# Kernel tuning notes

Measured on AMD Instinct MI355X. Metric: run time of the kernel, lower is better.

## Reference

```python
import jax, jax.numpy as jnp
import numpy as np

N_NODES = 100000
N_EDGES = 1600000
N_GRAPHS = 2048
HID = 64
IN_F = 14
N_CLS = 2
EPS = 1e-5


def _gcn_conv(x, row, col, w_edge, W, b, n_nodes):
    # PyG GCNConv with add_self_loops=True, normalize=True.
    xw = x @ W  # [N, out]
    # degree on target nodes, self-loop contributes weight 1
    deg = jnp.zeros((n_nodes,), x.dtype).at[col].add(w_edge) + 1.0
    dinv = deg ** -0.5
    norm = dinv[row] * w_edge * dinv[col]  # [E]
    out = jnp.zeros_like(xw).at[col].add(norm[:, None] * xw[row])
    out = out + (dinv * dinv)[:, None] * xw  # self-loop term
    return out + b


def _bn_relu(x, gamma, beta):
    mean = jnp.mean(x, axis=0)
    var = jnp.var(x, axis=0)  # biased, as PyTorch BN training normalization
    y = gamma * (x - mean) * jax.lax.rsqrt(var + EPS) + beta
    return jax.nn.relu(y)


def setup_inputs() -> dict:
    key = jax.random.key(0)
    ks = jax.random.split(key, 8)
    x = jax.random.normal(ks[0], (N_NODES, IN_F), dtype=jnp.float32)
    edge_index = jax.random.randint(ks[1], (2, N_EDGES), 0, N_NODES, dtype=jnp.int64)
    batch = jnp.sort(jax.random.randint(ks[2], (N_NODES,), 0, N_GRAPHS, dtype=jnp.int64))
    edge_weight = jnp.ones((N_EDGES,), dtype=jnp.float32)
    def lin(k, fi, fo):
        s = 1.0 / np.sqrt(fi)
        kw, kb = jax.random.split(k)
        return (jax.random.uniform(kw, (fi, fo), jnp.float32, -s, s),
                jax.random.uniform(kb, (fo,), jnp.float32, -s, s))
    W1, b1 = lin(ks[3], IN_F, HID)
    W2, b2 = lin(ks[4], HID, HID)
    W3, b3 = lin(ks[5], HID, HID)
    fcW, fcb = lin(ks[6], HID, N_CLS)
    g = jnp.ones((HID,), jnp.float32)
    z = jnp.zeros((HID,), jnp.float32)
    return {
        "x": x, "edge_index": edge_index, "batch": batch, "edge_weight": edge_weight,
        "W1": W1, "b1": b1, "W2": W2, "b2": b2, "W3": W3, "b3": b3,
        "g1": g, "bt1": z, "g2": g, "bt2": z, "g3": g, "bt3": z,
        "fcW": fcW, "fcb": fcb,
    }


def reference(x, edge_index, batch, edge_weight, W1, b1, W2, b2, W3, b3,
              g1, bt1, g2, bt2, g3, bt3, fcW, fcb):
    row, col = edge_index[0], edge_index[1]
    n = x.shape[0]
    h = _bn_relu(_gcn_conv(x, row, col, edge_weight, W1, b1, n), g1, bt1)
    h = _bn_relu(_gcn_conv(h, row, col, edge_weight, W2, b2, n), g2, bt2)
    h = _bn_relu(_gcn_conv(h, row, col, edge_weight, W3, b3, n), g3, bt3)
    node_embs = h  # dropout p=0 is identity
    graph_emb = jax.ops.segment_sum(node_embs, batch, num_segments=N_GRAPHS)
    out = graph_emb @ fcW + fcb
    return (out, node_embs, graph_emb)
```

## Files before the change

### kernel.cpp

```cpp
#include <hip/hip_runtime.h>
#include <hip/hip_fp16.h>

#define N_NODES 100000
#define N_EDGES 1600000
#define EMAX4   1900000
#define N_GRAPHS 2048
#define HID 64
#define IN_F 14
#define N_CLS 2
#define EPS 1e-5f

#define BSHIFT 9
#define NBUCK 196
#define ABLOCKS 256
#define CHUNK (N_EDGES / ABLOCKS)

#define NBLK2 128
#define NCHUNK2 ((N_NODES + NBLK2 - 1) / NBLK2)

typedef _Float16 half_t;
typedef _Float16 half8 __attribute__((ext_vector_type(8)));
typedef float f32x4 __attribute__((ext_vector_type(4)));
typedef unsigned int u32;
typedef u32 u32x4 __attribute__((ext_vector_type(4)));
typedef u32 u32x2 __attribute__((ext_vector_type(2)));

#define GSTRIDE ((size_t)N_NODES * 16)

__device__ __forceinline__ __half2 u32_as_half2(u32 u) {
    union { u32 u; __half2 h; } c;
    c.u = u;
    return c.h;
}


__global__ __launch_bounds__(256) void histA_kernel(const int* __restrict__ col,
                                                    int* __restrict__ histG) {
    __shared__ int hl[NBUCK];
    for (int i = threadIdx.x; i < NBUCK; i += 256) hl[i] = 0;
    __syncthreads();
    int e0 = blockIdx.x * CHUNK;
    for (int e = e0 + threadIdx.x; e < e0 + CHUNK; e += 256)
        atomicAdd(&hl[col[e] >> BSHIFT], 1);
    __syncthreads();
    for (int i = threadIdx.x; i < NBUCK; i += 256)
        histG[i * ABLOCKS + blockIdx.x] = hl[i];
}

__global__ __launch_bounds__(256) void scanS1_kernel(const int* __restrict__ histG,
                                                     int* __restrict__ bsumA) {
    __shared__ int ls[256];
    ls[threadIdx.x] = histG[blockIdx.x * 256 + threadIdx.x];
    __syncthreads();
    for (int off = 128; off > 0; off >>= 1) {
        if (threadIdx.x < off) ls[threadIdx.x] += ls[threadIdx.x + off];
        __syncthreads();
    }
    if (threadIdx.x == 0) bsumA[blockIdx.x] = ls[0];
}

__global__ __launch_bounds__(512) void topscan_kernel(int* __restrict__ bsum, int nb) {
    __shared__ int ls[512];
    int t = threadIdx.x;
    int v = (t < nb) ? bsum[t] : 0;
    ls[t] = v;
    __syncthreads();
    for (int off = 1; off < 512; off <<= 1) {
        int x = ls[t];
        if (t >= off) x += ls[t - off];
        __syncthreads();
        ls[t] = x;
        __syncthreads();
    }
    if (t < nb) bsum[t] = ls[t] - v;
}

__global__ __launch_bounds__(256) void scanS3_kernel(int* __restrict__ histG,
                                                     const int* __restrict__ bsumA,
                                                     int* __restrict__ ptr) {
    __shared__ int ls[256];
    int idx = blockIdx.x * 256 + threadIdx.x;
    int v = histG[idx];
    ls[threadIdx.x] = v;
    __syncthreads();
    for (int off = 1; off < 256; off <<= 1) {
        int x = ls[threadIdx.x];
        if (threadIdx.x >= off) x += ls[threadIdx.x - off];
        __syncthreads();
        ls[threadIdx.x] = x;
        __syncthreads();
    }
    histG[idx] = ls[threadIdx.x] - v + bsumA[blockIdx.x];
    if (blockIdx.x == 0 && threadIdx.x == 0) ptr[N_NODES] = N_EDGES;
}

__global__ __launch_bounds__(256) void scatterA_kernel(const int* __restrict__ row,
                                                       const int* __restrict__ col,
                                                       const float* __restrict__ w,
                                                       const int* __restrict__ histG,
                                                       int2* __restrict__ EA) {
    __shared__ int cur[NBUCK];
    for (int i = threadIdx.x; i < NBUCK; i += 256)
        cur[i] = histG[i * ABLOCKS + blockIdx.x];
    __syncthreads();
    int e0 = blockIdx.x * CHUNK;
    for (int e = e0 + threadIdx.x; e < e0 + CHUNK; e += 256) {
        int c = col[e];
        int r = row[e];
        int fx = (int)__float2uint_rn(w[e] * 8192.0f);
        int pos = atomicAdd(&cur[c >> BSHIFT], 1);
        EA[pos] = make_int2(r, (fx << 17) | c);
    }
}

__global__ __launch_bounds__(256) void bucketA_kernel(const int2* __restrict__ EA,
                                                      const int* __restrict__ bsumA,
                                                      int* __restrict__ ptr,
                                                      float* __restrict__ dinv) {
    __shared__ int hist[512], wsum[512];
    int b = blockIdx.x;
    int beg = bsumA[b];
    int end = (b == NBUCK - 1) ? N_EDGES : bsumA[b + 1];
    int i0 = threadIdx.x, i1 = threadIdx.x + 256;
    hist[i0] = 0; hist[i1] = 0;
    wsum[i0] = 0; wsum[i1] = 0;
    __syncthreads();
    for (int e = beg + threadIdx.x; e < end; e += 256) {
        int2 ed = EA[e];
        int c9 = ed.y & 511;
        atomicAdd(&hist[c9], 1);
        atomicAdd(&wsum[c9], (int)((unsigned int)ed.y >> 17));
    }
    __syncthreads();
    int cnt0 = hist[i0], cnt1 = hist[i1];
    for (int off = 1; off < 512; off <<= 1) {
        int v0 = hist[i0], v1 = hist[i1];
        int a0 = (i0 >= off) ? hist[i0 - off] : 0;
        int a1 = (i1 >= off) ? hist[i1 - off] : 0;
        __syncthreads();
        hist[i0] = v0 + a0;
        hist[i1] = v1 + a1;
        __syncthreads();
    }
    int excl0 = hist[i0] - cnt0, excl1 = hist[i1] - cnt1;
    int col0 = (b << BSHIFT) + i0, col1 = (b << BSHIFT) + i1;
    if (col0 < N_NODES) {
        ptr[col0] = beg + excl0;
        dinv[col0] = rsqrtf(1.0f + (float)wsum[i0] * (1.0f / 8192.0f));
    }
    if (col1 < N_NODES) {
        ptr[col1] = beg + excl1;
        dinv[col1] = rsqrtf(1.0f + (float)wsum[i1] * (1.0f / 8192.0f));
    }
}


__global__ __launch_bounds__(256) void histD_kernel(const int* __restrict__ ptr,
                                                    int* __restrict__ histD) {
    __shared__ int hl[2048];
    for (int i = threadIdx.x; i < 2048; i += 256) hl[i] = 0;
    __syncthreads();
    int n0 = blockIdx.x * NCHUNK2;
    int n1 = n0 + NCHUNK2; if (n1 > N_NODES) n1 = N_NODES;
    for (int n = n0 + threadIdx.x; n < n1; n += 256) {
        int d = ptr[n + 1] - ptr[n];
        if (d > 255) d = 255;
        atomicAdd(&hl[((threadIdx.x & 7) << 8) + d], 1);
    }
    __syncthreads();
    int s = 0;
#pragma unroll
    for (int c = 0; c < 8; c++) s += hl[(c << 8) + threadIdx.x];
    histD[threadIdx.x * NBLK2 + blockIdx.x] = s;
}

__global__ __launch_bounds__(128) void scanD1_kernel(const int* __restrict__ histD,
                                                     int* __restrict__ rowTot) {
    __shared__ int ls[128];
    ls[threadIdx.x] = histD[blockIdx.x * NBLK2 + threadIdx.x];
    __syncthreads();
    for (int off = 64; off > 0; off >>= 1) {
        if (threadIdx.x < off) ls[threadIdx.x] += ls[threadIdx.x + off];
        __syncthreads();
    }
    if (threadIdx.x == 0) rowTot[blockIdx.x] = ls[0];
}

__global__ __launch_bounds__(256) void topscanD_kernel(const int* __restrict__ rowTot,
                                                       int* __restrict__ nodeExcl,
                                                       int* __restrict__ edgeExcl,
                                                       int* __restrict__ ptrS) {
    __shared__ int a[256], b[256];
    int t = threadIdx.x;
    int cnt = rowTot[t];
    int dpad = (t + 3) & ~3;
    int ec = cnt * dpad;
    a[t] = cnt; b[t] = ec;
    __syncthreads();
    for (int off = 1; off < 256; off <<= 1) {
        int va = a[t], vb = b[t];
        if (t >= off) { va += a[t - off]; vb += b[t - off]; }
        __syncthreads();
        a[t] = va; b[t] = vb;
        __syncthreads();
    }
    nodeExcl[t] = a[t] - cnt;
    edgeExcl[t] = b[t] - ec;
    if (t == 255) ptrS[N_NODES] = b[255];
}

__global__ __launch_bounds__(128) void scanD3_kernel(int* __restrict__ histD,
                                                     const int* __restrict__ nodeExcl) {
    __shared__ int ls[128];
    int idx = blockIdx.x * NBLK2 + threadIdx.x;
    int v = histD[idx];
    ls[threadIdx.x] = v;
    __syncthreads();
    for (int off = 1; off < 128; off <<= 1) {
        int x = ls[threadIdx.x];
        if (threadIdx.x >= off) x += ls[threadIdx.x - off];
        __syncthreads();
        ls[threadIdx.x] = x;
        __syncthreads();
    }
    histD[idx] = ls[threadIdx.x] - v + nodeExcl[blockIdx.x];
}

__global__ __launch_bounds__(256) void scatterD_kernel(const int* __restrict__ ptr,
                                                       const int* __restrict__ histD,
                                                       const int* __restrict__ nodeExcl,
                                                       const int* __restrict__ edgeExcl,
                                                       int* __restrict__ perm,
                                                       int* __restrict__ ptrS,
                                                       int* __restrict__ newbase) {
    __shared__ int cur[256];
    cur[threadIdx.x] = histD[threadIdx.x * NBLK2 + blockIdx.x];
    __syncthreads();
    int n0 = blockIdx.x * NCHUNK2;
    int n1 = n0 + NCHUNK2; if (n1 > N_NODES) n1 = N_NODES;
    for (int n = n0 + threadIdx.x; n < n1; n += 256) {
        int d = ptr[n + 1] - ptr[n];
        if (d > 255) d = 255;
        int dpad = (d + 3) & ~3;
        int pos = atomicAdd(&cur[d], 1);
        int ebase = edgeExcl[d] + (pos - nodeExcl[d]) * dpad;
        perm[pos] = n;
        ptrS[pos] = ebase;
        newbase[n] = ebase;
    }
}

__global__ __launch_bounds__(256) void bucketB_kernel(const int2* __restrict__ EA,
                                                      const int* __restrict__ bsumA,
                                                      const int* __restrict__ newbase,
                                                      const float* __restrict__ dinv,
                                                      unsigned int* __restrict__ srcoff,
                                                      half_t* __restrict__ normh) {
    __shared__ int cur[512];
    int b = blockIdx.x;
    int beg = bsumA[b];
    int end = (b == NBUCK - 1) ? N_EDGES : bsumA[b + 1];
    int i0 = threadIdx.x, i1 = threadIdx.x + 256;
    int col0 = (b << BSHIFT) + i0, col1 = (b << BSHIFT) + i1;
    cur[i0] = (col0 < N_NODES) ? newbase[col0] : 0;
    cur[i1] = (col1 < N_NODES) ? newbase[col1] : 0;
    __syncthreads();
    for (int e = beg + threadIdx.x; e < end; e += 256) {
        int2 ed = EA[e];
        int c = ed.y & 0x1ffff;
        float w = (float)((unsigned int)ed.y >> 17) * (1.0f / 8192.0f);
        float nrm = dinv[ed.x] * w * dinv[c];
        int pos = atomicAdd(&cur[c & 511], 1);
        srcoff[pos] = (unsigned int)ed.x << 5;
        normh[pos] = (half_t)nrm;
    }
}


template <int K>
__global__ __launch_bounds__(256) void gemm_kernel(const float* __restrict__ h,
                                                   const float* __restrict__ W,
                                                   half_t* __restrict__ xw, int n_nodes) {
    int f = threadIdx.x & 63;
    float wcol[K];
#pragma unroll
    for (int k = 0; k < K; k++) wcol[k] = W[k * HID + f];
    half_t* xg = xw + (size_t)(f >> 4) * GSTRIDE + (f & 15);
    int wave = (blockIdx.x * blockDim.x + threadIdx.x) >> 6;
    int nwaves = (gridDim.x * blockDim.x) >> 6;
    for (int n = wave; n < n_nodes; n += nwaves) {
        const float* hr = h + (size_t)n * K;
        float acc = 0.f;
#pragma unroll
        for (int k = 0; k < K; k++) acc += hr[k] * wcol[k];
        xg[(size_t)n * 16] = (half_t)acc;
    }
}

__global__ __launch_bounds__(256) void gemm_bn_mfma_kernel(const half_t* __restrict__ h,
                                                           const float* __restrict__ W,
                                                           const float* __restrict__ stats,
                                                           const float* __restrict__ gamma,
                                                           const float* __restrict__ beta,
                                                           half_t* __restrict__ xw, int n_nodes) {
    __shared__ float sc_s[HID], sh_s[HID];
    if (threadIdx.x < 64) {
        float mean = stats[threadIdx.x] * (1.0f / N_NODES);
        float var = stats[64 + threadIdx.x] * (1.0f / N_NODES) - mean * mean;
        float sc = gamma[threadIdx.x] * rsqrtf(var + EPS);
        sc_s[threadIdx.x] = sc;
        sh_s[threadIdx.x] = beta[threadIdx.x] - mean * sc;
    }
    __syncthreads();
    int lane = threadIdx.x & 63;
    int col16 = lane & 15;
    int quad = lane >> 4;

    float scA[2][8], shA[2][8];
#pragma unroll
    for (int kh = 0; kh < 2; kh++)
#pragma unroll
        for (int j = 0; j < 8; j++) {
            int k = kh * 32 + quad * 8 + j;
            scA[kh][j] = sc_s[k];
            shA[kh][j] = sh_s[k];
        }

    half8 bfrag[4][2];
#pragma unroll
    for (int t = 0; t < 4; t++)
#pragma unroll
        for (int kh = 0; kh < 2; kh++)
#pragma unroll
            for (int j = 0; j < 8; j++) {
                int k = kh * 32 + quad * 8 + j;
                bfrag[t][kh][j] = (half_t)W[k * HID + t * 16 + col16];
            }

    int wave = (blockIdx.x * blockDim.x + threadIdx.x) >> 6;
    int nwaves = (gridDim.x * blockDim.x) >> 6;
    int ntiles = n_nodes >> 4;
    for (int tIdx = wave; tIdx < ntiles; tIdx += nwaves) {
        int n0 = tIdx << 4;
        half8 afrag[2];
#pragma unroll
        for (int kh = 0; kh < 2; kh++) {
            int k0 = kh * 32 + quad * 8;
            const half_t* hp = h + (size_t)(k0 >> 4) * GSTRIDE
                                 + (size_t)(n0 + col16) * 16 + (k0 & 15);
            half8 raw = *(const half8*)hp;
#pragma unroll
            for (int j = 0; j < 8; j++) {
                float v = (float)raw[j] * scA[kh][j] + shA[kh][j];
                afrag[kh][j] = (half_t)fmaxf(v, 0.f);
            }
        }
        f32x4 acc[4];
#pragma unroll
        for (int t = 0; t < 4; t++) {
            f32x4 z = {0.f, 0.f, 0.f, 0.f};
            acc[t] = __builtin_amdgcn_mfma_f32_16x16x32_f16(afrag[0], bfrag[t][0], z, 0, 0, 0);
            acc[t] = __builtin_amdgcn_mfma_f32_16x16x32_f16(afrag[1], bfrag[t][1], acc[t], 0, 0, 0);
        }
#pragma unroll
        for (int t = 0; t < 4; t++) {
            half_t* xg = xw + (size_t)t * GSTRIDE;
#pragma unroll
            for (int r = 0; r < 4; r++) {
                int rowi = n0 + quad * 4 + r;
                xg[(size_t)rowi * 16 + col16] = (half_t)acc[t][r];
            }
        }
    }
}

template <bool LAST>
__global__ __launch_bounds__(256) void gather_stats_kernel(const int* __restrict__ ptrS,
                                                           const int* __restrict__ perm,
                                                           const unsigned int* __restrict__ srcoff,
                                                           const half_t* __restrict__ normh,
                                                           const half_t* __restrict__ xw,
                                                           const float* __restrict__ dinv,
                                                           const float* __restrict__ b,
                                                           half_t* __restrict__ hp,
                                                           float* __restrict__ hf,
                                                           float* __restrict__ stats,
                                                           int n_nodes) {
    int g = (blockIdx.x & 7) >> 1;
    int grank = ((blockIdx.x >> 3) << 1) | (blockIdx.x & 1);
    int lane16 = threadIdx.x & 15;
    int quadLocal = threadIdx.x >> 4;
    int quadId = grank * 16 + quadLocal;
    int nquads = (gridDim.x >> 2) * 16;

    const half_t* xg = xw + (size_t)g * GSTRIDE;
    const char* xgc = (const char*)xg;
    unsigned int loff = (unsigned int)(lane16 * 2);
    const unsigned int* np = (const unsigned int*)normh;
    half_t* hpg = hp + (size_t)g * GSTRIDE;
    int f = g * 16 + lane16;
    float bf = b[f];

    float s = 0.f, s2 = 0.f;
    for (int i = quadId; i < n_nodes; i += nquads) {
        int node = perm[i];
        int j = ptrS[i];
        int cend = ptrS[i + 1];
        __half2 z2 = __float2half2_rn(0.f);
        __half2 acc0 = z2, acc1 = z2, acc2 = z2, acc3 = z2;
        for (; j + 16 <= cend; j += 16) {
            u32x4 s0 = *(const u32x4*)(srcoff + j);
            u32x4 s1 = *(const u32x4*)(srcoff + j + 4);
            u32x4 s2v = *(const u32x4*)(srcoff + j + 8);
            u32x4 s3 = *(const u32x4*)(srcoff + j + 12);
            int jh = j >> 1;
            u32x2 n0 = *(const u32x2*)(np + jh);
            u32x2 n1 = *(const u32x2*)(np + jh + 2);
            u32x2 n2 = *(const u32x2*)(np + jh + 4);
            u32x2 n3 = *(const u32x2*)(np + jh + 6);
            __half h0 = *(const __half*)(xgc + (s0.x + loff));
            __half h1 = *(const __half*)(xgc + (s0.y + loff));
            __half h2 = *(const __half*)(xgc + (s0.z + loff));
            __half h3 = *(const __half*)(xgc + (s0.w + loff));
            __half h4 = *(const __half*)(xgc + (s1.x + loff));
            __half h5 = *(const __half*)(xgc + (s1.y + loff));
            __half h6 = *(const __half*)(xgc + (s1.z + loff));
            __half h7 = *(const __half*)(xgc + (s1.w + loff));
            __half h8 = *(const __half*)(xgc + (s2v.x + loff));
            __half h9 = *(const __half*)(xgc + (s2v.y + loff));
            __half hA = *(const __half*)(xgc + (s2v.z + loff));
            __half hB = *(const __half*)(xgc + (s2v.w + loff));
            __half hC = *(const __half*)(xgc + (s3.x + loff));
            __half hD = *(const __half*)(xgc + (s3.y + loff));
            __half hE = *(const __half*)(xgc + (s3.z + loff));
            __half hF = *(const __half*)(xgc + (s3.w + loff));
            acc0 = __hfma2(u32_as_half2(n0.x), __halves2half2(h0, h1), acc0);
            acc0 = __hfma2(u32_as_half2(n0.y), __halves2half2(h2, h3), acc0);
            acc1 = __hfma2(u32_as_half2(n1.x), __halves2half2(h4, h5), acc1);
            acc1 = __hfma2(u32_as_half2(n1.y), __halves2half2(h6, h7), acc1);
            acc2 = __hfma2(u32_as_half2(n2.x), __halves2half2(h8, h9), acc2);
            acc2 = __hfma2(u32_as_half2(n2.y), __halves2half2(hA, hB), acc2);
            acc3 = __hfma2(u32_as_half2(n3.x), __halves2half2(hC, hD), acc3);
            acc3 = __hfma2(u32_as_half2(n3.y), __halves2half2(hE, hF), acc3);
        }
        for (; j < cend; j += 4) {
            u32x4 s0 = *(const u32x4*)(srcoff + j);
            u32x2 n0 = *(const u32x2*)(np + (j >> 1));
            __half h0 = *(const __half*)(xgc + (s0.x + loff));
            __half h1 = *(const __half*)(xgc + (s0.y + loff));
            __half h2 = *(const __half*)(xgc + (s0.z + loff));
            __half h3 = *(const __half*)(xgc + (s0.w + loff));
            acc0 = __hfma2(u32_as_half2(n0.x), __halves2half2(h0, h1), acc0);
            acc1 = __hfma2(u32_as_half2(n0.y), __halves2half2(h2, h3), acc1);
        }
        __half2 accp = __hadd2(__hadd2(acc0, acc1), __hadd2(acc2, acc3));
        float accf = __low2float(accp) + __high2float(accp);
        float di = dinv[node];
        float v = accf + di * di * (float)xg[(size_t)node * 16 + lane16] + bf;
        if (LAST)
            hf[(size_t)node * HID + f] = v;
        else
            hpg[(size_t)node * 16 + lane16] = (half_t)v;
        s += v;
        s2 += v * v;
    }
    __shared__ float ls[256], ls2[256];
    ls[threadIdx.x] = s;
    ls2[threadIdx.x] = s2;
    __syncthreads();
    if (threadIdx.x < 16) {
        float a = 0.f, aa = 0.f;
#pragma unroll
        for (int k = 0; k < 16; k++) {
            a += ls[k * 16 + threadIdx.x];
            aa += ls2[k * 16 + threadIdx.x];
        }
        atomicAdd(&stats[g * 16 + threadIdx.x], a);
        atomicAdd(&stats[64 + g * 16 + threadIdx.x], aa);
    }
}

__global__ __launch_bounds__(256) void bn_relu_seg_kernel(float* __restrict__ h,
                                                          const float* __restrict__ stats,
                                                          const float* __restrict__ gamma,
                                                          const float* __restrict__ beta,
                                                          const int* __restrict__ batch,
                                                          float* __restrict__ gemb,
                                                          int n_nodes) {
    int g = blockIdx.x * blockDim.x + threadIdx.x;
    int f = g & 63;
    int wave = g >> 6;
    int nwaves = (gridDim.x * blockDim.x) >> 6;
    int chunk = (n_nodes + nwaves - 1) / nwaves;
    int n0 = wave * chunk;
    int n1 = n0 + chunk;
    if (n1 > n_nodes) n1 = n_nodes;
    if (n0 >= n_nodes) return;
    float mean = stats[f] * (1.0f / N_NODES);
    float var = stats[64 + f] * (1.0f / N_NODES) - mean * mean;
    float sc = gamma[f] * rsqrtf(var + EPS);
    float sh = beta[f] - mean * sc;
    int curg = batch[n0];
    float racc = 0.f;
    for (int n = n0; n < n1; n++) {
        int bg = batch[n];
        if (bg != curg) {
            atomicAdd(&gemb[(size_t)curg * HID + f], racc);
            racc = 0.f;
            curg = bg;
        }
        size_t idx = (size_t)n * HID + f;
        float v = h[idx] * sc + sh;
        v = fmaxf(v, 0.f);
        h[idx] = v;
        racc += v;
    }
    atomicAdd(&gemb[(size_t)curg * HID + f], racc);
}

__global__ __launch_bounds__(256) void final_kernel(const float* __restrict__ gemb,
                                                    const float* __restrict__ fcW,
                                                    const float* __restrict__ fcb,
                                                    float* __restrict__ out) {
    int g = blockIdx.x * blockDim.x + threadIdx.x;
    if (g >= N_GRAPHS * N_CLS) return;
    int gr = g >> 1, c = g & 1;
    float acc = fcb[c];
#pragma unroll
    for (int k = 0; k < HID; k++) acc += gemb[gr * HID + k] * fcW[k * N_CLS + c];
    out[g] = acc;
}


extern "C" void kernel_launch(void* const* d_in, const int* in_sizes, int n_in,
                              void* d_out, int out_size, void* d_ws, size_t ws_size,
                              hipStream_t stream) {
    const float* x    = (const float*)d_in[0];
    const int*   ei   = (const int*)d_in[1];
    const int*   batch= (const int*)d_in[2];
    const float* ew   = (const float*)d_in[3];
    const float* W1   = (const float*)d_in[4];
    const float* b1   = (const float*)d_in[5];
    const float* W2   = (const float*)d_in[6];
    const float* b2   = (const float*)d_in[7];
    const float* W3   = (const float*)d_in[8];
    const float* b3   = (const float*)d_in[9];
    const float* g1   = (const float*)d_in[10];
    const float* bt1  = (const float*)d_in[11];
    const float* g2   = (const float*)d_in[12];
    const float* bt2  = (const float*)d_in[13];
    const float* g3   = (const float*)d_in[14];
    const float* bt3  = (const float*)d_in[15];
    const float* fcW  = (const float*)d_in[16];
    const float* fcb  = (const float*)d_in[17];

    const int* row = ei;
    const int* col = ei + N_EDGES;

    float* out_head  = (float*)d_out;
    float* node_embs = out_head + N_GRAPHS * N_CLS;
    float* gemb      = node_embs + (size_t)N_NODES * HID;

    char* bse = (char*)d_ws;
    half_t* xwh = (half_t*)bse;
    char* r1 = bse + (size_t)N_NODES * HID * 2;
    int2*   EA  = (int2*)r1;
    half_t* hpl = (half_t*)r1;
    char* r2 = r1 + (size_t)N_NODES * HID * 2;
    unsigned int* srcoff = (unsigned int*)r2;
    half_t* normh = (half_t*)(srcoff + EMAX4);
    char* r3 = r2 + (size_t)EMAX4 * 6;
    float* dinv  = (float*)r3;
    float* stats3 = dinv + N_NODES;
    int*   ptr   = (int*)(stats3 + 384);
    int*   histG = ptr + N_NODES + 1;
    int*   bsumA = histG + NBUCK * ABLOCKS;
    int*   histD = bsumA + NBUCK + 4;
    int*   rowTot = histD + 256 * NBLK2;
    int*   nodeExcl = rowTot + 256;
    int*   edgeExcl = nodeExcl + 256;
    int*   perm   = edgeExcl + 256;
    int*   newbase= perm + N_NODES;
    int*   ptrS   = newbase + N_NODES;

    const int B   = 256;
    const int gGS = 1024;
    const int gGA = 2048;

    histA_kernel<<<ABLOCKS, B, 0, stream>>>(col, histG);
    scanS1_kernel<<<NBUCK, B, 0, stream>>>(histG, bsumA);
    topscan_kernel<<<1, 512, 0, stream>>>(bsumA, NBUCK);
    scanS3_kernel<<<NBUCK, B, 0, stream>>>(histG, bsumA, ptr);
    scatterA_kernel<<<ABLOCKS, B, 0, stream>>>(row, col, ew, histG, EA);
    bucketA_kernel<<<NBUCK, B, 0, stream>>>(EA, bsumA, ptr, dinv);

    histD_kernel<<<NBLK2, B, 0, stream>>>(ptr, histD);
    scanD1_kernel<<<256, 128, 0, stream>>>(histD, rowTot);
    topscanD_kernel<<<1, 256, 0, stream>>>(rowTot, nodeExcl, edgeExcl, ptrS);
    scanD3_kernel<<<256, 128, 0, stream>>>(histD, nodeExcl);
    scatterD_kernel<<<NBLK2, B, 0, stream>>>(ptr, histD, nodeExcl, edgeExcl,
                                             perm, ptrS, newbase);
    hipMemsetAsync(srcoff, 0, (size_t)EMAX4 * 6, stream);
    hipMemsetAsync(stats3, 0, 384 * sizeof(float), stream);
    hipMemsetAsync(gemb, 0, (size_t)N_GRAPHS * HID * sizeof(float), stream);
    bucketB_kernel<<<NBUCK, B, 0, stream>>>(EA, bsumA, newbase, dinv, srcoff, normh);

    float* h3 = node_embs;

    gemm_kernel<IN_F><<<gGS, B, 0, stream>>>(x, W1, xwh, N_NODES);
    gather_stats_kernel<false><<<gGA, B, 0, stream>>>(ptrS, perm, srcoff, normh, xwh,
                                                      dinv, b1, hpl, h3, stats3, N_NODES);

    gemm_bn_mfma_kernel<<<gGS, B, 0, stream>>>(hpl, W2, stats3, g1, bt1, xwh, N_NODES);
    gather_stats_kernel<false><<<gGA, B, 0, stream>>>(ptrS, perm, srcoff, normh, xwh,
                                                      dinv, b2, hpl, h3, stats3 + 128, N_NODES);

    gemm_bn_mfma_kernel<<<gGS, B, 0, stream>>>(hpl, W3, stats3 + 128, g2, bt2, xwh, N_NODES);
    gather_stats_kernel<true><<<gGA, B, 0, stream>>>(ptrS, perm, srcoff, normh, xwh,
                                                     dinv, b3, hpl, h3, stats3 + 256, N_NODES);

    bn_relu_seg_kernel<<<gGS, B, 0, stream>>>(h3, stats3 + 256, g3, bt3, batch, gemb, N_NODES);

    final_kernel<<<(N_GRAPHS * N_CLS + B - 1) / B, B, 0, stream>>>(gemb, fcW, fcb, out_head);
}
```

Measured before the change: 432.8 us.

## Switch feature layout from 4 feature groups to row-major, wave-per-node gather with fp32 accumulation

Replaces the group-major layout (four planes of 16 fp16 features per node) with plain row-major [N,64] fp16. Each wave now gathers all 64 features of a node at once, so every edge fetches one contiguous 128-byte row instead of four 32-byte pieces handled by separate blocks. The edge index is read once per node instead of once per group. Accumulation moves from packed half2 FMA to fp32 with eight accumulators, which costs more ALU work and conversions in exchange for better precision.

```diff
diff --git a/kernel.cpp b/kernel.cpp
--- a/kernel.cpp
+++ b/kernel.cpp
@@ -24,8 +24,6 @@
 typedef unsigned int u32;
 typedef u32 u32x4 __attribute__((ext_vector_type(4)));
 typedef u32 u32x2 __attribute__((ext_vector_type(2)));
-
-#define GSTRIDE ((size_t)N_NODES * 16)
 
 __device__ __forceinline__ __half2 u32_as_half2(u32 u) {
     union { u32 u; __half2 h; } c;
@@ -271,7 +269,7 @@
         float w = (float)((unsigned int)ed.y >> 17) * (1.0f / 8192.0f);
         float nrm = dinv[ed.x] * w * dinv[c];
         int pos = atomicAdd(&cur[c & 511], 1);
-        srcoff[pos] = (unsigned int)ed.x << 5;
+        srcoff[pos] = (unsigned int)ed.x << 7;
         normh[pos] = (half_t)nrm;
     }
 }
@@ -285,7 +283,6 @@
     float wcol[K];
 #pragma unroll
     for (int k = 0; k < K; k++) wcol[k] = W[k * HID + f];
-    half_t* xg = xw + (size_t)(f >> 4) * GSTRIDE + (f & 15);
     int wave = (blockIdx.x * blockDim.x + threadIdx.x) >> 6;
     int nwaves = (gridDim.x * blockDim.x) >> 6;
     for (int n = wave; n < n_nodes; n += nwaves) {
@@ -293,7 +290,7 @@
         float acc = 0.f;
 #pragma unroll
         for (int k = 0; k < K; k++) acc += hr[k] * wcol[k];
-        xg[(size_t)n * 16] = (half_t)acc;
+        xw[(size_t)n * HID + f] = (half_t)acc;
     }
 }
 
@@ -345,9 +342,7 @@
         half8 afrag[2];
 #pragma unroll
         for (int kh = 0; kh < 2; kh++) {
-            int k0 = kh * 32 + quad * 8;
-            const half_t* hp = h + (size_t)(k0 >> 4) * GSTRIDE
-                                 + (size_t)(n0 + col16) * 16 + (k0 & 15);
+            const half_t* hp = h + (size_t)(n0 + col16) * HID + kh * 32 + quad * 8;
             half8 raw = *(const half8*)hp;
 #pragma unroll
             for (int j = 0; j < 8; j++) {
@@ -363,14 +358,12 @@
             acc[t] = __builtin_amdgcn_mfma_f32_16x16x32_f16(afrag[1], bfrag[t][1], acc[t], 0, 0, 0);
         }
 #pragma unroll
-        for (int t = 0; t < 4; t++) {
-            half_t* xg = xw + (size_t)t * GSTRIDE;
+        for (int t = 0; t < 4; t++)
 #pragma unroll
             for (int r = 0; r < 4; r++) {
                 int rowi = n0 + quad * 4 + r;
-                xg[(size_t)rowi * 16 + col16] = (half_t)acc[t][r];
+                xw[(size_t)rowi * HID + t * 16 + col16] = (half_t)acc[t][r];
             }
-        }
     }
 }
 
@@ -386,81 +379,78 @@
                                                            float* __restrict__ hf,
                                                            float* __restrict__ stats,
                                                            int n_nodes) {
-    int g = (blockIdx.x & 7) >> 1;
-    int grank = ((blockIdx.x >> 3) << 1) | (blockIdx.x & 1);
-    int lane16 = threadIdx.x & 15;
-    int quadLocal = threadIdx.x >> 4;
-    int quadId = grank * 16 + quadLocal;
-    int nquads = (gridDim.x >> 2) * 16;
-
-    const half_t* xg = xw + (size_t)g * GSTRIDE;
-    const char* xgc = (const char*)xg;
-    unsigned int loff = (unsigned int)(lane16 * 2);
+    int lane = threadIdx.x & 63;
+    int waveId = (blockIdx.x * blockDim.x + threadIdx.x) >> 6;
+    int nwaves = (gridDim.x * blockDim.x) >> 6;
+
+    const char* xgc = (const char*)xw;
+    unsigned int loff = (unsigned int)(lane * 2);
     const unsigned int* np = (const unsigned int*)normh;
-    half_t* hpg = hp + (size_t)g * GSTRIDE;
-    int f = g * 16 + lane16;
-    float bf = b[f];
+    float bf = b[lane];
 
     float s = 0.f, s2 = 0.f;
-    for (int i = quadId; i < n_nodes; i += nquads) {
+    for (int i = waveId; i < n_nodes; i += nwaves) {
         int node = perm[i];
         int j = ptrS[i];
         int cend = ptrS[i + 1];
-        __half2 z2 = __float2half2_rn(0.f);
-        __half2 acc0 = z2, acc1 = z2, acc2 = z2, acc3 = z2;
+        float a0 = 0.f, a1 = 0.f, a2 = 0.f, a3 = 0.f;
+        float a4 = 0.f, a5 = 0.f, a6 = 0.f, a7 = 0.f;
         for (; j + 16 <= cend; j += 16) {
             u32x4 s0 = *(const u32x4*)(srcoff + j);
             u32x4 s1 = *(const u32x4*)(srcoff + j + 4);
             u32x4 s2v = *(const u32x4*)(srcoff + j + 8);
             u32x4 s3 = *(const u32x4*)(srcoff + j + 12);
             int jh = j >> 1;
-            u32x2 n0 = *(const u32x2*)(np + jh);
-            u32x2 n1 = *(const u32x2*)(np + jh + 2);
-            u32x2 n2 = *(const u32x2*)(np + jh + 4);
-            u32x2 n3 = *(const u32x2*)(np + jh + 6);
-            __half h0 = *(const __half*)(xgc + (s0.x + loff));
-            __half h1 = *(const __half*)(xgc + (s0.y + loff));
-            __half h2 = *(const __half*)(xgc + (s0.z + loff));
-            __half h3 = *(const __half*)(xgc + (s0.w + loff));
-            __half h4 = *(const __half*)(xgc + (s1.x + loff));
-            __half h5 = *(const __half*)(xgc + (s1.y + loff));
-            __half h6 = *(const __half*)(xgc + (s1.z + loff));
-            __half h7 = *(const __half*)(xgc + (s1.w + loff));
-            __half h8 = *(const __half*)(xgc + (s2v.x + loff));
-            __half h9 = *(const __half*)(xgc + (s2v.y + loff));
-            __half hA = *(const __half*)(xgc + (s2v.z + loff));
-            __half hB = *(const __half*)(xgc + (s2v.w + loff));
-            __half hC = *(const __half*)(xgc + (s3.x + loff));
-            __half hD = *(const __half*)(xgc + (s3.y + loff));
-            __half hE = *(const __half*)(xgc + (s3.z + loff));
-            __half hF = *(const __half*)(xgc + (s3.w + loff));
-            acc0 = __hfma2(u32_as_half2(n0.x), __halves2half2(h0, h1), acc0);
-            acc0 = __hfma2(u32_as_half2(n0.y), __halves2half2(h2, h3), acc0);
-            acc1 = __hfma2(u32_as_half2(n1.x), __halves2half2(h4, h5), acc1);
-            acc1 = __hfma2(u32_as_half2(n1.y), __halves2half2(h6, h7), acc1);
-            acc2 = __hfma2(u32_as_half2(n2.x), __halves2half2(h8, h9), acc2);
-            acc2 = __hfma2(u32_as_half2(n2.y), __halves2half2(hA, hB), acc2);
-            acc3 = __hfma2(u32_as_half2(n3.x), __halves2half2(hC, hD), acc3);
-            acc3 = __hfma2(u32_as_half2(n3.y), __halves2half2(hE, hF), acc3);
+            u32x4 nA = *(const u32x4*)(np + jh);
+            u32x4 nB = *(const u32x4*)(np + jh + 4);
+            float x0 = (float)*(const __half*)(xgc + (s0.x + loff));
+            float x1 = (float)*(const __half*)(xgc + (s0.y + loff));
+            float x2 = (float)*(const __half*)(xgc + (s0.z + loff));
+            float x3 = (float)*(const __half*)(xgc + (s0.w + loff));
+            float x4 = (float)*(const __half*)(xgc + (s1.x + loff));
+            float x5 = (float)*(const __half*)(xgc + (s1.y + loff));
+            float x6 = (float)*(const __half*)(xgc + (s1.z + loff));
+            float x7 = (float)*(const __half*)(xgc + (s1.w + loff));
+            float x8 = (float)*(const __half*)(xgc + (s2v.x + loff));
+            float x9 = (float)*(const __half*)(xgc + (s2v.y + loff));
+            float xA = (float)*(const __half*)(xgc + (s2v.z + loff));
+            float xB = (float)*(const __half*)(xgc + (s2v.w + loff));
+            float xC = (float)*(const __half*)(xgc + (s3.x + loff));
+            float xD = (float)*(const __half*)(xgc + (s3.y + loff));
+            float xE = (float)*(const __half*)(xgc + (s3.z + loff));
+            float xF = (float)*(const __half*)(xgc + (s3.w + loff));
+            __half2 n0h = u32_as_half2(nA.x), n1h = u32_as_half2(nA.y);
+            __half2 n2h = u32_as_half2(nA.z), n3h = u32_as_half2(nA.w);
+            __half2 n4h = u32_as_half2(nB.x), n5h = u32_as_half2(nB.y);
+            __half2 n6h = u32_as_half2(nB.z), n7h = u32_as_half2(nB.w);
+            a0 += __low2float(n0h) * x0;  a1 += __high2float(n0h) * x1;
+            a2 += __low2float(n1h) * x2;  a3 += __high2float(n1h) * x3;
+            a4 += __low2float(n2h) * x4;  a5 += __high2float(n2h) * x5;
+            a6 += __low2float(n3h) * x6;  a7 += __high2float(n3h) * x7;
+            a0 += __low2float(n4h) * x8;  a1 += __high2float(n4h) * x9;
+            a2 += __low2float(n5h) * xA;  a3 += __high2float(n5h) * xB;
+            a4 += __low2float(n6h) * xC;  a5 += __high2float(n6h) * xD;
+            a6 += __low2float(n7h) * xE;  a7 += __high2float(n7h) * xF;
         }
         for (; j < cend; j += 4) {
             u32x4 s0 = *(const u32x4*)(srcoff + j);
             u32x2 n0 = *(const u32x2*)(np + (j >> 1));
-            __half h0 = *(const __half*)(xgc + (s0.x + loff));
-            __half h1 = *(const __half*)(xgc + (s0.y + loff));
-            __half h2 = *(const __half*)(xgc + (s0.z + loff));
-            __half h3 = *(const __half*)(xgc + (s0.w + loff));
-            acc0 = __hfma2(u32_as_half2(n0.x), __halves2half2(h0, h1), acc0);
-            acc1 = __hfma2(u32_as_half2(n0.y), __halves2half2(h2, h3), acc1);
+            float x0 = (float)*(const __half*)(xgc + (s0.x + loff));
+            float x1 = (float)*(const __half*)(xgc + (s0.y + loff));
+            float x2 = (float)*(const __half*)(xgc + (s0.z + loff));
+            float x3 = (float)*(const __half*)(xgc + (s0.w + loff));
+            __half2 n0h = u32_as_half2(n0.x), n1h = u32_as_half2(n0.y);
+            a0 += __low2float(n0h) * x0;  a1 += __high2float(n0h) * x1;
+            a2 += __low2float(n1h) * x2;  a3 += __high2float(n1h) * x3;
         }
-        __half2 accp = __hadd2(__hadd2(acc0, acc1), __hadd2(acc2, acc3));
-        float accf = __low2float(accp) + __high2float(accp);
+        float accf = (((a0 + a1) + (a2 + a3)) + ((a4 + a5) + (a6 + a7)));
         float di = dinv[node];
-        float v = accf + di * di * (float)xg[(size_t)node * 16 + lane16] + bf;
+        float xself = (float)*(const __half*)(xgc + (((unsigned int)node << 7) + loff));
+        float v = accf + di * di * xself + bf;
         if (LAST)
-            hf[(size_t)node * HID + f] = v;
+            hf[(size_t)node * HID + lane] = v;
         else
-            hpg[(size_t)node * 16 + lane16] = (half_t)v;
+            hp[(size_t)node * HID + lane] = (half_t)v;
         s += v;
         s2 += v * v;
     }
@@ -468,15 +458,11 @@
     ls[threadIdx.x] = s;
     ls2[threadIdx.x] = s2;
     __syncthreads();
-    if (threadIdx.x < 16) {
-        float a = 0.f, aa = 0.f;
-#pragma unroll
-        for (int k = 0; k < 16; k++) {
-            a += ls[k * 16 + threadIdx.x];
-            aa += ls2[k * 16 + threadIdx.x];
-        }
-        atomicAdd(&stats[g * 16 + threadIdx.x], a);
-        atomicAdd(&stats[64 + g * 16 + threadIdx.x], aa);
+    if (threadIdx.x < 64) {
+        float a = ls[threadIdx.x] + ls[threadIdx.x + 64] + ls[threadIdx.x + 128] + ls[threadIdx.x + 192];
+        float aa = ls2[threadIdx.x] + ls2[threadIdx.x + 64] + ls2[threadIdx.x + 128] + ls2[threadIdx.x + 192];
+        atomicAdd(&stats[threadIdx.x], a);
+        atomicAdd(&stats[64 + threadIdx.x], aa);
     }
 }
 
```

Result: slower. 506.6 us (+17.0%).
